# Optimization experiments

Hardware: AMD Instinct MI355X
Metric: run time of the kernel (lower is better)

## Reference

```python
import jax, jax.numpy as jnp
import numpy as np

TAU_MEM = 20.0
TAU_SYN = 5.0
THRESHOLD = 1.0
SURROGATE_BETA = 4.0
RESET_POTENTIAL = 0.0

B, T, D_IN, H = 32, 1024, 512, 512


def setup_inputs() -> dict:
    key = jax.random.key(0)
    k1, k2 = jax.random.split(key)
    inputs = jax.random.normal(k1, (B, T, D_IN), dtype=jnp.float32)
    kernel = jax.random.normal(k2, (D_IN, H), dtype=jnp.float32) / np.sqrt(D_IN)
    bias = jnp.zeros((H,), dtype=jnp.float32)
    return {"inputs": inputs, "kernel": kernel, "bias": bias}


def reference(inputs, kernel, bias):
    batch = inputs.shape[0]
    hidden = kernel.shape[1]
    alpha_mem = jnp.exp(jnp.float32(-1.0 / TAU_MEM))
    alpha_syn = jnp.exp(jnp.float32(-1.0 / TAU_SYN))

    # Batch the per-step dense GEMM across time: [B,T,Din] @ [Din,H] -> [B,T,H]
    currents = jnp.einsum('bti,ih->bth', inputs, kernel) + bias
    currents_t = jnp.swapaxes(currents, 0, 1)  # [T,B,H] for scan

    def step(carry, ic):
        v_mem, i_syn = carry
        i_syn = alpha_syn * i_syn + ic
        v_mem = alpha_mem * v_mem + (1.0 - alpha_mem) * i_syn
        spikes = (v_mem >= THRESHOLD).astype(jnp.float32)
        surrogate = SURROGATE_BETA / (2.0 * (1.0 + jnp.cosh(SURROGATE_BETA * (v_mem - THRESHOLD))))
        spikes_with_grad = spikes + jax.lax.stop_gradient(spikes - surrogate)
        v_mem = jnp.where(spikes > 0, RESET_POTENTIAL, v_mem)
        return (v_mem, i_syn), (spikes_with_grad, v_mem)

    init = (jnp.zeros((batch, hidden), jnp.float32), jnp.zeros((batch, hidden), jnp.float32))
    (v_final, _), (spikes_t, vmem_t) = jax.lax.scan(step, init, currents_t)

    spike_output = jnp.swapaxes(spikes_t, 0, 1)      # [B,T,H]
    membrane_states = jnp.swapaxes(vmem_t, 0, 1)     # [B,T,H]
    spike_rate = jnp.mean(spike_output)
    return spike_output, membrane_states, v_final, spike_rate
```

## Files before the change

### kernel.cpp

```cpp
#include <hip/hip_runtime.h>

typedef unsigned short ushort_t;
typedef unsigned int   uint_t;
typedef float    float4v __attribute__((ext_vector_type(4)));
typedef _Float16 h16x8   __attribute__((ext_vector_type(8)));

#define Bsz 32
#define Tsz 1024
#define Din 512
#define Hsz 512
#define Mtot (Bsz * Tsz)
#define ELEMS ((size_t)Mtot * Hsz)

#define GLL16(gp, lp) __builtin_amdgcn_global_load_lds(                        \
    (const __attribute__((address_space(1))) unsigned int*)(gp),               \
    (__attribute__((address_space(3))) unsigned int*)(lp), 16, 0, 0)

#define GLL4(gp, lp) __builtin_amdgcn_global_load_lds(                         \
    (const __attribute__((address_space(1))) unsigned int*)(gp),               \
    (__attribute__((address_space(3))) unsigned int*)(lp), 4, 0, 0)

__global__ __launch_bounds__(256) void split_fp16x2(
    const float* __restrict__ A, const float* __restrict__ W,
    _Float16* __restrict__ Ah, _Float16* __restrict__ Bh)
{
    const int bid = blockIdx.x, tid = threadIdx.x;
    if (bid < 4096) {
        const size_t e   = ((size_t)bid * 256 + tid) * 16;
        const int    row = (int)(e >> 9);
        const int    col = (int)(e & 511);
        const float4* Af = (const float4*)(A + e);
        h16x8 v0a, v1a, v0b, v1b;
#pragma unroll
        for (int q = 0; q < 4; ++q) {
            float4 x = Af[q];
            const float c[4] = {x.x, x.y, x.z, x.w};
#pragma unroll
            for (int j = 0; j < 4; ++j) {
                const float xs = c[j] * 256.0f;
                const _Float16 h0 = (_Float16)xs;
                const float rf = xs - (float)h0;
                const _Float16 h1 = (_Float16)rf;
                const int idx = q * 4 + j;
                if (idx < 8) { v0a[idx] = h0; v1a[idx] = h1; }
                else         { v0b[idx - 8] = h0; v1b[idx - 8] = h1; }
            }
        }
        _Float16* d0 = Ah + (size_t)row * 1024 + col;
        *(h16x8*)(d0)           = v0a;
        *(h16x8*)(d0 + 8)       = v0b;
        *(h16x8*)(d0 + 512)     = v1a;
        *(h16x8*)(d0 + 512 + 8) = v1b;
    } else {
        const int f4 = (bid - 4096) * 256 + tid;
        const int k  = f4 >> 7;
        const int n4 = (f4 & 127) << 2;
        float4 x = *(const float4*)(W + (size_t)k * Hsz + n4);
        const float c[4] = {x.x, x.y, x.z, x.w};
#pragma unroll
        for (int j = 0; j < 4; ++j) {
            const float ws = c[j] * 2048.0f;
            const _Float16 h0 = (_Float16)ws;
            const float rf = ws - (float)h0;
            const _Float16 h1 = (_Float16)rf;
            _Float16* d = Bh + (size_t)(n4 + j) * 1024 + k;
            d[0]   = h0;
            d[512] = h1;
        }
    }
}

#define SA_STAGE(LIMB, KK, SLOTBASE) do {                                      \
    const char* g_ = Ag + (size_t)((LIMB) * 1024) + (size_t)((KK) * 64);       \
    _Pragma("unroll") for (int H = 0; H < 4; ++H)                              \
        GLL16(g_ + (size_t)H * 131072, ldsA + (SLOTBASE) + H * 4096 + lsd);    \
} while (0)

#define SB_STAGE(LIMB, KK, SLOT) do {                                          \
    const char* g_ = Bg + (size_t)((LIMB) * 1024) + (size_t)((KK) * 64);       \
    _Pragma("unroll") for (int H = 0; H < 2; ++H)                              \
        GLL16(g_ + (size_t)H * 131072, ldsB + (SLOT) * 8192 + H * 4096 + lsd); \
} while (0)

#define LD_AF(SLOTBASE) do {                                                   \
    _Pragma("unroll") for (int mf = 0; mf < 8; ++mf)                           \
        af[mf] = *(const h16x8*)(ldsA + (SLOTBASE) + (wm + mf * 16 + lr) * 64  \
                                 + physf * 16);                                \
} while (0)

#define LD_BF(DST, SLOT) do {                                                  \
    _Pragma("unroll") for (int nf = 0; nf < 4; ++nf)                           \
        DST[nf] = *(const h16x8*)(ldsB + (SLOT) * 8192 + (wn + nf * 16 + lr)   \
                                  * 64 + physf * 16);                          \
} while (0)

#define MFMAH(BF) do { __builtin_amdgcn_s_setprio(1);                          \
    _Pragma("unroll") for (int mf = 0; mf < 8; ++mf)                           \
    _Pragma("unroll") for (int nf = 0; nf < 4; ++nf)                           \
        acc[mf][nf] = __builtin_amdgcn_mfma_f32_16x16x32_f16(                  \
            af[mf], BF[nf], acc[mf][nf], 0, 0, 0);                             \
    __builtin_amdgcn_s_setprio(0); } while (0)

#define GATE(N) do { asm volatile("s_waitcnt vmcnt(" #N ")" ::: "memory");     \
    __builtin_amdgcn_sched_barrier(0); __builtin_amdgcn_s_barrier();           \
    asm volatile("" ::: "memory"); } while (0)

__global__ __launch_bounds__(256, 2) void gemm_f16k3(
    const _Float16* __restrict__ Ah, const _Float16* __restrict__ Bh,
    const float* __restrict__ bias, float* __restrict__ C)
{
    __shared__ __align__(16) char lds[65536];
    char* ldsA = lds;
    char* ldsB = lds + 32768;

    const int tid = threadIdx.x;
    const int bid = blockIdx.x;
    const int lin = ((bid & 7) << 6) | (bid >> 3);
    const int m0  = (lin >> 2) << 8;
    const int n0  = (lin & 3) << 7;
    const int w = tid >> 6, lane = tid & 63;
    const int wm = (w & 1) << 7;
    const int wn = (w >> 1) << 6;
    const int lr = lane & 15, lg = lane >> 4;

    const int physf = lg ^ (lr & 3) ^ ((lr >> 2) & 3);

    const int srow = tid >> 2;
    const int schk = tid & 3;
    const int logchk = schk ^ (srow & 3) ^ ((srow >> 2) & 3);
    const int lsd = tid * 16;
    const char* Ag = (const char*)Ah + (size_t)(m0 + srow) * 2048 + logchk * 16;
    const char* Bg = (const char*)Bh + (size_t)(n0 + srow) * 2048 + logchk * 16;

    float4v acc[8][4];
#pragma unroll
    for (int i = 0; i < 8; ++i)
#pragma unroll
        for (int j = 0; j < 4; ++j) acc[i][j] = (float4v)0.f;

    h16x8 af[8], bf0[4], bf1[4];

    SA_STAGE(0, 0, 0);
    SB_STAGE(0, 0, 0); SB_STAGE(1, 0, 1);
    SB_STAGE(0, 1, 2); SB_STAGE(1, 1, 3);
    GATE(0);

#pragma unroll 1
    for (int k = 0; k < 15; ++k) {
        const int s0 = (2 * k) & 3, s1 = (2 * k + 1) & 3;
        GATE(4);
        LD_AF(0); LD_BF(bf0, s0);
        SA_STAGE(1, k, 16384);
        MFMAH(bf0);
        GATE(4);
        LD_BF(bf1, s1);
        SA_STAGE(0, k + 1, 0);
        MFMAH(bf1);
        GATE(4);
        LD_AF(16384);
        if (k < 14) { SB_STAGE(0, k + 2, s0); SB_STAGE(1, k + 2, s1); }
        MFMAH(bf0);
    }
    {
        GATE(0);
        LD_AF(0); LD_BF(bf0, 2);
        SA_STAGE(1, 15, 16384);
        MFMAH(bf0);
        GATE(4);
        LD_BF(bf1, 3);
        MFMAH(bf1);
        GATE(0);
        LD_AF(16384);
        MFMAH(bf0);
    }

    constexpr float INVS = 1.0f / 524288.0f;
#pragma unroll
    for (int nf = 0; nf < 4; ++nf) {
        const int col = n0 + wn + nf * 16 + lr;
        const float bv = bias[col];
#pragma unroll
        for (int mf = 0; mf < 8; ++mf)
#pragma unroll
            for (int j = 0; j < 4; ++j) {
                const int row = m0 + wm + mf * 16 + lg * 4 + j;
                C[(size_t)row * Hsz + col] = fmaf(acc[mf][nf][j], INVS, bv);
            }
    }
}

#define BM 128
#define BN 128
#define BK 16
#define LDSA (BM + 4)
#define LDSB (BN + 4)
__global__ __launch_bounds__(256) void sgemm_currents(
    const float* __restrict__ A, const float* __restrict__ B,
    const float* __restrict__ bias, float* __restrict__ C)
{
    __shared__ float As[BK][LDSA];
    __shared__ float Bs[BK][LDSB];
    const int tid = threadIdx.x;
    const int tx = tid & 15, ty = tid >> 4;
    const int m0 = blockIdx.y * BM, n0 = blockIdx.x * BN;
    const int arow = tid >> 2, ac4 = (tid & 3) * 4;
    const int brow = tid >> 5, bc4 = (tid & 31) * 4;
    float acc[8][8];
#pragma unroll
    for (int i = 0; i < 8; ++i)
#pragma unroll
        for (int j = 0; j < 8; ++j) acc[i][j] = 0.f;
    const float* Abase = A + (size_t)(m0 + arow) * Din + ac4;
    const float* Bbase = B + (size_t)brow * Hsz + n0 + bc4;
    float4 a0 = *(const float4*)Abase;
    float4 a1 = *(const float4*)(Abase + (size_t)64 * Din);
    float4 b0 = *(const float4*)Bbase;
    float4 b1 = *(const float4*)(Bbase + (size_t)8 * Hsz);
    const int NKT = Din / BK;
    for (int kt = 0; kt < NKT; ++kt) {
        const float* apf = (const float*)&a0;
        const float* aqf = (const float*)&a1;
#pragma unroll
        for (int j = 0; j < 4; ++j) As[ac4 + j][arow] = apf[j];
#pragma unroll
        for (int j = 0; j < 4; ++j) As[ac4 + j][arow + 64] = aqf[j];
        *(float4*)&Bs[brow][bc4] = b0;
        *(float4*)&Bs[brow + 8][bc4] = b1;
        __syncthreads();
        if (kt + 1 < NKT) {
            const float* An = Abase + (kt + 1) * BK;
            const float* Bn = Bbase + (size_t)(kt + 1) * BK * Hsz;
            a0 = *(const float4*)An;
            a1 = *(const float4*)(An + (size_t)64 * Din);
            b0 = *(const float4*)Bn;
            b1 = *(const float4*)(Bn + (size_t)8 * Hsz);
        }
#pragma unroll
        for (int k = 0; k < BK; ++k) {
            float4 af0 = *(const float4*)&As[k][ty * 8];
            float4 af1 = *(const float4*)&As[k][ty * 8 + 4];
            float4 bf0 = *(const float4*)&Bs[k][tx * 8];
            float4 bf1 = *(const float4*)&Bs[k][tx * 8 + 4];
            const float av[8] = {af0.x, af0.y, af0.z, af0.w, af1.x, af1.y, af1.z, af1.w};
            const float bv[8] = {bf0.x, bf0.y, bf0.z, bf0.w, bf1.x, bf1.y, bf1.z, bf1.w};
#pragma unroll
            for (int i = 0; i < 8; ++i)
#pragma unroll
                for (int j = 0; j < 8; ++j) acc[i][j] = fmaf(av[i], bv[j], acc[i][j]);
        }
        __syncthreads();
    }
    const float4 bi0 = *(const float4*)&bias[n0 + tx * 8];
    const float4 bi1 = *(const float4*)&bias[n0 + tx * 8 + 4];
#pragma unroll
    for (int i = 0; i < 8; ++i) {
        const size_t row = (size_t)(m0 + ty * 8 + i);
        float4 o0 = make_float4(acc[i][0] + bi0.x, acc[i][1] + bi0.y,
                                acc[i][2] + bi0.z, acc[i][3] + bi0.w);
        float4 o1 = make_float4(acc[i][4] + bi1.x, acc[i][5] + bi1.y,
                                acc[i][6] + bi1.z, acc[i][7] + bi1.w);
        float* cp = C + row * Hsz + n0 + tx * 8;
        *(float4*)cp = o0;
        *(float4*)(cp + 4) = o1;
    }
}

__global__ __launch_bounds__(256) void lif_scan_pc(
    const float* __restrict__ cur, float* __restrict__ spikes,
    float* __restrict__ vmem, float* __restrict__ vfinal,
    float* __restrict__ partials)
{
    __shared__ __align__(16) float lbuf[2][32][64];
    __shared__ __align__(16) float pbuf[2][32][64];

    constexpr float A_M  = 0.95122942450071400910f;
    constexpr float OM_M = 1.0f - A_M;
    constexpr float A_S  = 0.81873075307798182354f;

    const int tid  = threadIdx.x;
    const int lane = tid & 63;
    const int wv   = tid >> 6;
    const int bid  = blockIdx.x;
    const int batch = bid >> 3;
    const int hbase = (bid & 7) << 6;
    const size_t sbase = (size_t)batch * (size_t)(Tsz * Hsz) + hbase + lane;

    if (wv == 0) {
        const float* gsrc = cur + sbase;
#pragma unroll
        for (int r = 0; r < 32; ++r)
            GLL4(gsrc + r * 512, &lbuf[0][r][0]);
        asm volatile("s_waitcnt vmcnt(0)" ::: "memory");
        __builtin_amdgcn_sched_barrier(0);

        float v = 0.f, isyn = 0.f;
#pragma unroll 1
        for (int c = 0; c < 32; ++c) {
            if (c < 31) {
                const float* gs = gsrc + (size_t)(c + 1) * 16384;
                float (*db)[64] = lbuf[(c + 1) & 1];
#pragma unroll
                for (int r = 0; r < 32; ++r)
                    GLL4(gs + r * 512, &db[r][0]);
            }
            const float* lrow = &lbuf[c & 1][0][lane];
            float* prow = &pbuf[c & 1][0][lane];
#pragma unroll
            for (int r = 0; r < 32; ++r) {
                isyn = fmaf(A_S, isyn, lrow[r * 64]);
                v    = fmaf(A_M, v, OM_M * isyn);
                prow[r * 64] = v;
                v = (v >= 1.0f) ? 0.0f : v;
            }
            asm volatile("s_waitcnt vmcnt(0) lgkmcnt(0)" ::: "memory");
            __builtin_amdgcn_sched_barrier(0);
            __builtin_amdgcn_s_barrier();
            asm volatile("" ::: "memory");
        }
        vfinal[bid * 64 + lane] = v;
        __builtin_amdgcn_s_barrier();
    } else {
        const int cj = wv - 1;
        const int r0 = cj * 11;
        const int rn = (cj == 2) ? 10 : 11;
        float* gspk = spikes + sbase;
        float* gvmm = vmem + sbase;
        float acc = 0.f;

        __builtin_amdgcn_s_barrier();
        asm volatile("" ::: "memory");
#pragma unroll 1
        for (int c = 0; c < 32; ++c) {
            const float* prow = &pbuf[c & 1][0][lane];
            float* sp = gspk + (size_t)c * 16384;
            float* vp = gvmm + (size_t)c * 16384;
#pragma unroll
            for (int k = 0; k < 11; ++k) {
                if (k < rn) {
                    const int r = r0 + k;
                    const float pv = prow[r * 64];
                    const bool sb = (pv >= 1.0f);
                    float x = fminf(fmaf(4.0f, pv, -4.0f), 30.0f);
                    const float ep = __expf(x);
                    const float tt = 1.0f + ep;
                    const float rr = __builtin_amdgcn_rcpf(tt * tt);
                    const float s2 = sb ? 2.0f : 0.0f;
                    const float so = fmaf(-4.0f * ep, rr, s2);
                    const float vo = sb ? 0.0f : pv;
                    acc += so;
                    sp[r * 512] = so;
                    vp[r * 512] = vo;
                }
            }
            asm volatile("" ::: "memory");
            __builtin_amdgcn_s_barrier();
            asm volatile("" ::: "memory");
        }
#pragma unroll
        for (int o = 32; o; o >>= 1) acc += __shfl_down(acc, o);
        if (lane == 0) partials[cj * 256 + bid] = acc;
    }
}

__device__ __forceinline__ void lif_step(float c, float& v, float& isyn,
                                         float& so_out)
{
    constexpr float A_M  = 0.95122942450071400910f;
    constexpr float OM_M = 1.0f - A_M;
    constexpr float A_S  = 0.81873075307798182354f;
    isyn = fmaf(A_S, isyn, c);
    v    = fmaf(A_M, v, OM_M * isyn);
    const float sp = (v >= 1.0f) ? 1.0f : 0.0f;
    float x = fmaf(4.0f, v, -4.0f);
    x = fminf(x, 30.0f);
    const float ep = __expf(x);
    const float tt = 1.0f + ep;
    const float surr = 4.0f * ep * __builtin_amdgcn_rcpf(tt * tt);
    so_out = fmaf(2.0f, sp, -surr);
    v = (sp > 0.f) ? 0.0f : v;
}

__global__ __launch_bounds__(64) void lif_scan(
    const float* cur, float* spikes, float* vmem, float* vfinal, float* partials)
{
    const int tid = threadIdx.x;
    const int gid = blockIdx.x * 64 + tid;
    const size_t base = ((size_t)(gid >> 9)) * (size_t)Tsz * Hsz + (gid & 511);

    float v = 0.f, isyn = 0.f, acc = 0.f;
    constexpr int P = 8;
    float ring[P];
#pragma unroll
    for (int p = 0; p < P; ++p) ring[p] = cur[base + (size_t)p * Hsz];

    for (int t = 0; t < Tsz; t += P) {
#pragma unroll
        for (int p = 0; p < P; ++p) {
            const float c = ring[p];
            int tn = t + P + p;
            tn = tn < (Tsz - 1) ? tn : (Tsz - 1);
            ring[p] = cur[base + (size_t)tn * Hsz];

            float so;
            lif_step(c, v, isyn, so);
            const size_t idx = base + (size_t)(t + p) * Hsz;
            spikes[idx] = so;
            vmem[idx]   = v;
            acc += so;
        }
    }
    vfinal[gid] = v;
#pragma unroll
    for (int off = 32; off; off >>= 1) acc += __shfl_down(acc, off);
    if (tid == 0) partials[blockIdx.x] = acc;
}

__global__ __launch_bounds__(256) void rate_finalize(
    const float* __restrict__ partials, float* __restrict__ rate)
{
    const int tid = threadIdx.x;
    float s = partials[tid];
#pragma unroll
    for (int off = 32; off; off >>= 1) s += __shfl_down(s, off);
    __shared__ float wsum[4];
    if ((tid & 63) == 0) wsum[tid >> 6] = s;
    __syncthreads();
    if (tid == 0)
        rate[0] = ((wsum[0] + wsum[1]) + (wsum[2] + wsum[3])) * (1.0f / 16777216.0f);
}

__global__ __launch_bounds__(256) void rate_finalize3(
    const float* __restrict__ partials, float* __restrict__ rate)
{
    const int tid = threadIdx.x;
    float s = partials[tid] + partials[256 + tid] + partials[512 + tid];
#pragma unroll
    for (int off = 32; off; off >>= 1) s += __shfl_down(s, off);
    __shared__ float wsum[4];
    if ((tid & 63) == 0) wsum[tid >> 6] = s;
    __syncthreads();
    if (tid == 0)
        rate[0] = ((wsum[0] + wsum[1]) + (wsum[2] + wsum[3])) * (1.0f / 16777216.0f);
}

extern "C" void kernel_launch(void* const* d_in, const int* in_sizes, int n_in,
                              void* d_out, int out_size, void* d_ws, size_t ws_size,
                              hipStream_t stream)
{
    const float* inputs = (const float*)d_in[0];
    const float* weight = (const float*)d_in[1];
    const float* bias   = (const float*)d_in[2];

    float* out    = (float*)d_out;
    float* spikes = out;
    float* vmem   = out + ELEMS;
    float* vfinal = out + 2 * ELEMS;
    float* rate   = vfinal + (size_t)Bsz * Hsz;

    float* partials = (float*)d_ws;
    char*  ws       = (char*)d_ws;

    const size_t HDR   = 16384;
    const size_t CUR_B = ELEMS * 4;
    const size_t AH_B  = (size_t)Mtot * 1024 * 2;
    const size_t BH_B  = (size_t)Hsz * 1024 * 2;

    _Float16 *Ah, *Bh;
    float* cur;
    int path;
    if (ws_size >= HDR + CUR_B + AH_B + BH_B) {
        cur = (float*)(ws + HDR);
        Ah  = (_Float16*)(ws + HDR + CUR_B);
        Bh  = Ah + (size_t)Mtot * 1024;
        path = 0;
    } else if (ws_size >= HDR + CUR_B) {
        cur = (float*)(ws + HDR);
        Ah  = (_Float16*)d_out;
        Bh  = Ah + (size_t)Mtot * 1024;
        path = 1;
    } else {
        cur = vmem;
        Ah = Bh = nullptr;
        path = 2;
    }

    if (path != 2) {
        split_fp16x2<<<dim3(4096 + 256), 256, 0, stream>>>(inputs, weight, Ah, Bh);
        gemm_f16k3<<<dim3(512), 256, 0, stream>>>(Ah, Bh, bias, cur);
        lif_scan_pc<<<dim3(256), 256, 0, stream>>>(cur, spikes, vmem, vfinal, partials);
        rate_finalize3<<<dim3(1), 256, 0, stream>>>(partials, rate);
    } else {
        sgemm_currents<<<dim3(4, 256), 256, 0, stream>>>(inputs, weight, bias, cur);
        lif_scan<<<dim3(256), 64, 0, stream>>>(cur, spikes, vmem, vfinal, partials);
        rate_finalize<<<dim3(1), 256, 0, stream>>>(partials, rate);
    }
}
```

Measured before the change: 134.5 us.

## Triple-buffer A-tile LDS staging to deepen GEMM prefetch pipeline

Grows LDS from 64KB to 80KB so A chunks rotate through three slots instead of two. The main loop is restructured into groups of three k-steps, and A loads are issued two chunks ahead with looser vmcnt gates. The aim is to hide more global-load latency behind MFMA work. The extra LDS may lower occupancy below the two blocks per CU requested by the launch bounds, and the rotated slot indexing adds risk.

```diff
diff --git a/kernel.cpp b/kernel.cpp
--- a/kernel.cpp
+++ b/kernel.cpp
@@ -70,28 +70,30 @@
     }
 }
 
-#define SA_STAGE(LIMB, KK, SLOTBASE) do {                                      \
-    const char* g_ = Ag + (size_t)((LIMB) * 1024) + (size_t)((KK) * 64);       \
+#define SA_C(C, SLOT) do {                                                     \
+    const char* g_ = Ag + (size_t)((((C) & 1) * 1024) + (((C) >> 1) * 64));    \
+    char* l_ = ldsA + (SLOT) * 16384 + lsd;                                    \
     _Pragma("unroll") for (int H = 0; H < 4; ++H)                              \
-        GLL16(g_ + (size_t)H * 131072, ldsA + (SLOTBASE) + H * 4096 + lsd);    \
+        GLL16(g_ + (size_t)H * 131072, l_ + H * 4096);                         \
 } while (0)
 
-#define SB_STAGE(LIMB, KK, SLOT) do {                                          \
+#define SB_K(LIMB, KK, SLOT) do {                                              \
     const char* g_ = Bg + (size_t)((LIMB) * 1024) + (size_t)((KK) * 64);       \
+    char* l_ = ldsB + (SLOT) * 8192 + lsd;                                     \
     _Pragma("unroll") for (int H = 0; H < 2; ++H)                              \
-        GLL16(g_ + (size_t)H * 131072, ldsB + (SLOT) * 8192 + H * 4096 + lsd); \
+        GLL16(g_ + (size_t)H * 131072, l_ + H * 4096);                         \
 } while (0)
 
-#define LD_AF(SLOTBASE) do {                                                   \
+#define LD_AF(SLOT) do {                                                       \
     _Pragma("unroll") for (int mf = 0; mf < 8; ++mf)                           \
-        af[mf] = *(const h16x8*)(ldsA + (SLOTBASE) + (wm + mf * 16 + lr) * 64  \
-                                 + physf * 16);                                \
+        af[mf] = *(const h16x8*)(ldsA + (SLOT) * 16384 +                       \
+                                 (wm + mf * 16 + lr) * 64 + physf * 16);       \
 } while (0)
 
 #define LD_BF(DST, SLOT) do {                                                  \
     _Pragma("unroll") for (int nf = 0; nf < 4; ++nf)                           \
-        DST[nf] = *(const h16x8*)(ldsB + (SLOT) * 8192 + (wn + nf * 16 + lr)   \
-                                  * 64 + physf * 16);                          \
+        DST[nf] = *(const h16x8*)(ldsB + (SLOT) * 8192 +                       \
+                                  (wn + nf * 16 + lr) * 64 + physf * 16);      \
 } while (0)
 
 #define MFMAH(BF) do { __builtin_amdgcn_s_setprio(1);                          \
@@ -105,13 +107,32 @@
     __builtin_amdgcn_sched_barrier(0); __builtin_amdgcn_s_barrier();           \
     asm volatile("" ::: "memory"); } while (0)
 
+#define GROUP(K, PAR, SA0, SA2, SW0, SW2, STAGE_B) do {                        \
+    const int b0_ = (PAR) * 2, b1_ = (PAR) * 2 + 1;                            \
+                                                                       \
+    GATE(8);                                                                   \
+    LD_AF(SA0); LD_BF(bf0, b0_);                                               \
+    SA_C(2 * (K) + 2, SW0);                                                    \
+    MFMAH(bf0);                                                                \
+                                                                       \
+    GATE(12);                                                                  \
+    LD_BF(bf1, b1_);                                                           \
+    MFMAH(bf1);                                                                \
+                                                                       \
+    GATE(4);                                                                   \
+    LD_AF(SA2);                                                                \
+    SA_C(2 * (K) + 3, SW2);                                                    \
+    if (STAGE_B) { SB_K(0, (K) + 2, b0_); SB_K(1, (K) + 2, b1_); }             \
+    MFMAH(bf0);                                                                \
+} while (0)
+
 __global__ __launch_bounds__(256, 2) void gemm_f16k3(
     const _Float16* __restrict__ Ah, const _Float16* __restrict__ Bh,
     const float* __restrict__ bias, float* __restrict__ C)
 {
-    __shared__ __align__(16) char lds[65536];
+    __shared__ __align__(16) char lds[81920];
     char* ldsA = lds;
-    char* ldsB = lds + 32768;
+    char* ldsB = lds + 49152;
 
     const int tid = threadIdx.x;
     const int bid = blockIdx.x;
@@ -140,39 +161,33 @@
 
     h16x8 af[8], bf0[4], bf1[4];
 
-    SA_STAGE(0, 0, 0);
-    SB_STAGE(0, 0, 0); SB_STAGE(1, 0, 1);
-    SB_STAGE(0, 1, 2); SB_STAGE(1, 1, 3);
+    SA_C(0, 0); SA_C(1, 1);
+    SB_K(0, 0, 0); SB_K(1, 0, 1);
+    SB_K(0, 1, 2); SB_K(1, 1, 3);
     GATE(0);
 
 #pragma unroll 1
-    for (int k = 0; k < 15; ++k) {
-        const int s0 = (2 * k) & 3, s1 = (2 * k + 1) & 3;
+    for (int t = 0; t < 5; ++t) {
+        const int kpar = t & 1;
+        const int k0 = 3 * t;
+        GROUP(k0,     kpar,     0, 1, 2, 0, 1);
+        GROUP(k0 + 1, kpar ^ 1, 2, 0, 1, 2, 1);
+        GROUP(k0 + 2, kpar,     1, 2, 0, 1, (t < 4));
+    }
+
+    {
         GATE(4);
-        LD_AF(0); LD_BF(bf0, s0);
-        SA_STAGE(1, k, 16384);
-        MFMAH(bf0);
-        GATE(4);
-        LD_BF(bf1, s1);
-        SA_STAGE(0, k + 1, 0);
-        MFMAH(bf1);
-        GATE(4);
-        LD_AF(16384);
-        if (k < 14) { SB_STAGE(0, k + 2, s0); SB_STAGE(1, k + 2, s1); }
-        MFMAH(bf0);
-    }
-    {
-        GATE(0);
         LD_AF(0); LD_BF(bf0, 2);
-        SA_STAGE(1, 15, 16384);
         MFMAH(bf0);
         GATE(4);
         LD_BF(bf1, 3);
         MFMAH(bf1);
         GATE(0);
-        LD_AF(16384);
+        LD_AF(1);
         MFMAH(bf0);
     }
+    asm volatile("s_waitcnt vmcnt(0)" ::: "memory");
+    __builtin_amdgcn_sched_barrier(0);
 
     constexpr float INVS = 1.0f / 524288.0f;
 #pragma unroll
```

Result: no change. 136.7 us (+1.7%).
